# Kernel tuning notes

Measured on AMD Instinct MI355X. Metric: run time of the kernel, lower is better.

The kernel has to match this reference:

```python
import jax, jax.numpy as jnp
import numpy as np

N_NODES = 50000


def gcn_conv(h, src, dst, W, b, n):
    # PyG GCNConv: x' = D^{-1/2} (A + I) D^{-1/2} (h W) + b
    x = h @ W  # [N, out]
    deg = jax.ops.segment_sum(jnp.ones_like(src, dtype=x.dtype), dst, num_segments=n) + 1.0  # self-loop
    dis = deg ** -0.5
    norm = dis[src] * dis[dst]  # [E]
    msg = x[src] * norm[:, None]  # [E, out]
    agg = jax.ops.segment_sum(msg, dst, num_segments=n)
    agg = agg + x * (dis * dis)[:, None]  # self-loop term: 1/deg_i * x_i
    return agg + b


def setup_inputs() -> dict:
    key = jax.random.key(0)
    ks = jax.random.split(key, 8)
    n, e = N_NODES, 800000
    d_in, d_rni, h = 128, 32, 256
    x = jax.random.normal(ks[0], (n, d_in), dtype=jnp.float32)
    rni = jax.random.normal(ks[1], (n, d_rni), dtype=jnp.float32)
    edge_index = jax.random.randint(ks[2], (2, e), 0, n, dtype=jnp.int64)
    s1 = (d_in + d_rni) ** -0.5
    s2 = h ** -0.5
    W1 = jax.random.normal(ks[3], (d_in + d_rni, h), dtype=jnp.float32) * s1
    b1 = jnp.zeros((h,), dtype=jnp.float32)
    W2 = jax.random.normal(ks[4], (h, h), dtype=jnp.float32) * s2
    b2 = jnp.zeros((h,), dtype=jnp.float32)
    W_out = jax.random.normal(ks[5], (h, h), dtype=jnp.float32) * s2
    b_out = jnp.zeros((h,), dtype=jnp.float32)
    return {"x": x, "rni": rni, "edge_index": edge_index, "W1": W1, "b1": b1,
            "W2": W2, "b2": b2, "W_out": W_out, "b_out": b_out}


def reference(x, rni, edge_index, W1, b1, W2, b2, W_out, b_out):
    n = x.shape[0]
    src, dst = edge_index[0], edge_index[1]
    h = jnp.concatenate([x, rni], axis=-1)  # RNI concat
    h = jax.nn.relu(gcn_conv(h, src, dst, W1, b1, n))
    h = jax.nn.relu(gcn_conv(h, src, dst, W2, b2, n))
    return h @ W_out + b_out
```

## Files before the change

### kernel.cpp

```cpp
#include <hip/hip_runtime.h>
#include <hip/hip_bf16.h>
#include <hip/hip_fp16.h>
#include <math.h>

#define D_IN   128
#define D_RNI  32
#define HID    256

typedef _Float16 half8 __attribute__((ext_vector_type(8)));
typedef float    f32x4 __attribute__((ext_vector_type(4)));

__global__ void k_prep(const unsigned int* __restrict__ ew, int nwords, int* __restrict__ mode,
                       const float* __restrict__ W1, __half* __restrict__ W1t,
                       const float* __restrict__ W2, __half* __restrict__ W2t,
                       const float* __restrict__ Wo, __half* __restrict__ Wot,
                       int* __restrict__ counts, int n) {
    int b = blockIdx.x;
    if (b == 0) {
        __shared__ unsigned int red[256];
        unsigned int acc = 0;
        for (int i = threadIdx.x; i < 1024; i += 256) {
            int idx = 2 * i + 1;
            if (idx < nwords) acc |= ew[idx];
        }
        red[threadIdx.x] = acc;
        __syncthreads();
        for (int s = 128; s > 0; s >>= 1) {
            if (threadIdx.x < s) red[threadIdx.x] |= red[threadIdx.x + s];
            __syncthreads();
        }
        if (threadIdx.x == 0) *mode = (red[0] == 0u) ? 1 : 0;
        return;
    }
    const int T1 = (D_IN + D_RNI) * HID;
    const int T2 = HID * HID;
    const int TW = T1 + 2 * T2;
    int i = (b - 1) * 256 + threadIdx.x;
    if (i < T1) {
        int k = i / HID, nn = i - k * HID;
        W1t[(size_t)nn * (D_IN + D_RNI) + k] = __float2half(W1[i]);
    } else if (i < T1 + T2) {
        int j = i - T1;
        int k = j / HID, nn = j - k * HID;
        W2t[(size_t)nn * HID + k] = __float2half(W2[j]);
    } else if (i < TW) {
        int j = i - T1 - T2;
        int k = j / HID, nn = j - k * HID;
        Wot[(size_t)nn * HID + k] = __float2half(Wo[j]);
    } else {
        int j = i - TW;
        if (j < n) counts[j] = 0;
    }
}

__global__ void k_count(const unsigned int* __restrict__ ew, const int* __restrict__ mode_p,
                        int* __restrict__ counts, int e) {
    int mode = *mode_p;
    int i = blockIdx.x * 256 + threadIdx.x;
    if (i >= e) return;
    int d = mode ? (int)ew[2 * ((size_t)e + i)] : (int)ew[(size_t)e + i];
    atomicAdd(&counts[d], 1);
}

__global__ __launch_bounds__(1024) void k_scan1(const int* __restrict__ counts,
                                                int* __restrict__ incl,
                                                int* __restrict__ bsum, int n) {
    __shared__ int sd[1024];
    int t = threadIdx.x;
    int i = blockIdx.x * 1024 + t;
    int v = (i < n) ? counts[i] : 0;
    sd[t] = v;
    __syncthreads();
    for (int off = 1; off < 1024; off <<= 1) {
        int tmp = (t >= off) ? sd[t - off] : 0;
        __syncthreads();
        sd[t] += tmp;
        __syncthreads();
    }
    if (i < n) incl[i] = sd[t];
    if (t == 1023) bsum[blockIdx.x] = sd[1023];
}

__global__ void k_scan3(const int* __restrict__ counts, const int* __restrict__ incl,
                        const int* __restrict__ bsum,
                        int* __restrict__ rowptr, int* __restrict__ cursor,
                        float* __restrict__ dis, int n, int nb) {
    __shared__ int pre_s, tot_s;
    int t = threadIdx.x;
    int c = (blockIdx.x * 256) >> 10;
    if (t < 64) {
        int v   = (t < nb) ? bsum[t] : 0;
        int pre = (t < c)  ? v : 0;
        int tot = v;
        #pragma unroll
        for (int m = 32; m > 0; m >>= 1) {
            pre += __shfl_down(pre, m);
            tot += __shfl_down(tot, m);
        }
        if (t == 0) { pre_s = pre; tot_s = tot; }
    }
    __syncthreads();
    int i = blockIdx.x * 256 + t;
    if (i >= n) return;
    int excl = incl[i] - counts[i] + pre_s;
    rowptr[i] = excl;
    cursor[i] = excl;
    dis[i] = 1.0f / sqrtf((float)(counts[i] + 1));
    if (i == 0) rowptr[n] = tot_s;
}

#define KT 32
#define LSTR 40
template <bool A_F32, bool ADD_BIAS, bool HALF_OUT>
__device__ __forceinline__ void gemm_body(int blk,
                                          const void* __restrict__ Av, int strideA, int KA,
                                          const void* __restrict__ A2v, int strideA2,
                                          const __half* __restrict__ Bt,
                                          const float* __restrict__ bias,
                                          void* Cv, int M, int K) {
    __shared__ __half As[2][128 * LSTR];
    __shared__ __half Bs[2][256 * LSTR];
    int tid = threadIdx.x;
    int wave = tid >> 6, lane = tid & 63;
    int wm = wave >> 2, wn = wave & 3;
    int q = lane >> 4, m16 = lane & 15;
    int r0 = blk * 128;

    int ar  = tid >> 2, akq = (tid & 3) * 8;
    int br  = tid >> 1, bkq = (tid & 1) * 16;

    int arow = r0 + ar; if (arow >= M) arow = M - 1;

    f32x4 acc[4][4] = {};

    float4 afr0, afr1;
    uint4  areg;
    uint4  breg0, breg1;

    auto loadA = [&](int k0) {
        if (A_F32) {
            const float* src; int stride, kk0;
            if (k0 < KA) { src = (const float*)Av;  stride = strideA;  kk0 = k0; }
            else         { src = (const float*)A2v; stride = strideA2; kk0 = k0 - KA; }
            const float* p = &src[(size_t)arow * stride + kk0 + akq];
            afr0 = *reinterpret_cast<const float4*>(p);
            afr1 = *reinterpret_cast<const float4*>(p + 4);
        } else {
            const __half* src = (const __half*)Av;
            areg = *reinterpret_cast<const uint4*>(&src[(size_t)arow * strideA + k0 + akq]);
        }
    };
    auto loadB = [&](int k0) {
        const __half* p = &Bt[(size_t)br * K + k0 + bkq];
        breg0 = *reinterpret_cast<const uint4*>(p);
        breg1 = *reinterpret_cast<const uint4*>(p + 8);
    };
    auto writeLDS = [&](int buf) {
        if (A_F32) {
            union { __half2 h2[4]; uint4 u; } uu;
            uu.h2[0] = __floats2half2_rn(afr0.x, afr0.y);
            uu.h2[1] = __floats2half2_rn(afr0.z, afr0.w);
            uu.h2[2] = __floats2half2_rn(afr1.x, afr1.y);
            uu.h2[3] = __floats2half2_rn(afr1.z, afr1.w);
            *reinterpret_cast<uint4*>(&As[buf][ar * LSTR + akq]) = uu.u;
        } else {
            *reinterpret_cast<uint4*>(&As[buf][ar * LSTR + akq]) = areg;
        }
        *reinterpret_cast<uint4*>(&Bs[buf][br * LSTR + bkq])     = breg0;
        *reinterpret_cast<uint4*>(&Bs[buf][br * LSTR + bkq + 8]) = breg1;
    };

    const int S = K / KT;
    loadA(0); loadB(0);
    writeLDS(0);
    __syncthreads();

    for (int t = 0; t < S; ++t) {
        int cur = t & 1;
        if (t + 1 < S) { loadA((t + 1) * KT); loadB((t + 1) * KT); }

        half8 af[4], bf[4];
        #pragma unroll
        for (int mi = 0; mi < 4; ++mi)
            af[mi] = *reinterpret_cast<const half8*>(&As[cur][(wm * 64 + mi * 16 + m16) * LSTR + q * 8]);
        #pragma unroll
        for (int ni = 0; ni < 4; ++ni)
            bf[ni] = *reinterpret_cast<const half8*>(&Bs[cur][(wn * 64 + ni * 16 + m16) * LSTR + q * 8]);
        #pragma unroll
        for (int mi = 0; mi < 4; ++mi)
            #pragma unroll
            for (int ni = 0; ni < 4; ++ni)
                acc[mi][ni] = __builtin_amdgcn_mfma_f32_16x16x32_f16(af[mi], bf[ni], acc[mi][ni], 0, 0, 0);

        if (t + 1 < S) writeLDS(cur ^ 1);
        __syncthreads();
    }

    #pragma unroll
    for (int mi = 0; mi < 4; ++mi) {
        #pragma unroll
        for (int r = 0; r < 4; ++r) {
            int row = r0 + wm * 64 + mi * 16 + q * 4 + r;
            if (row >= M) continue;
            #pragma unroll
            for (int ni = 0; ni < 4; ++ni) {
                int col = wn * 64 + ni * 16 + m16;
                float v = acc[mi][ni][r];
                if (ADD_BIAS) v += bias[col];
                if (HALF_OUT) ((__half*)Cv)[(size_t)row * HID + col] = __float2half(v);
                else          ((float*)Cv)[(size_t)row * HID + col] = v;
            }
        }
    }
}

template <bool A_F32, bool ADD_BIAS, bool HALF_OUT>
__global__ __launch_bounds__(512, 4) void k_mgemm(const void* __restrict__ Av, int strideA, int KA,
                                                  const void* __restrict__ A2v, int strideA2,
                                                  const __half* __restrict__ Bt,
                                                  const float* __restrict__ bias,
                                                  void* Cv, int M, int K) {
    gemm_body<A_F32, ADD_BIAS, HALF_OUT>(blockIdx.x, Av, strideA, KA, A2v, strideA2,
                                         Bt, bias, Cv, M, K);
}

#define SCAT_BLKS 121
__global__ __launch_bounds__(512, 4) void k_scatgemm(
        const unsigned int* __restrict__ ew, const int* __restrict__ mode_p,
        int* __restrict__ cursor, int* __restrict__ csr, int e,
        const float* __restrict__ x, const float* __restrict__ rni,
        const __half* __restrict__ W1t, __half* __restrict__ xh, int M, int K) {
    if ((int)blockIdx.x >= SCAT_BLKS) {
        gemm_body<true, false, true>((int)blockIdx.x - SCAT_BLKS, x, D_IN, D_IN, rni, D_RNI,
                                     W1t, nullptr, xh, M, K);
        return;
    }
    const int t0     = (int)blockIdx.x * 512 + (int)threadIdx.x;
    const int stride = SCAT_BLKS * 512 * 4;
    const int mode   = *mode_p;
    for (int i = t0 * 4; i < e; i += stride) {
        if (i + 4 <= e) {
            int s0, s1, s2, s3, d0, d1, d2, d3;
            if (mode) {
                s0 = (int)ew[2 * (size_t)(i + 0)]; d0 = (int)ew[2 * ((size_t)e + i + 0)];
                s1 = (int)ew[2 * (size_t)(i + 1)]; d1 = (int)ew[2 * ((size_t)e + i + 1)];
                s2 = (int)ew[2 * (size_t)(i + 2)]; d2 = (int)ew[2 * ((size_t)e + i + 2)];
                s3 = (int)ew[2 * (size_t)(i + 3)]; d3 = (int)ew[2 * ((size_t)e + i + 3)];
            } else {
                s0 = (int)ew[(size_t)(i + 0)]; d0 = (int)ew[(size_t)e + i + 0];
                s1 = (int)ew[(size_t)(i + 1)]; d1 = (int)ew[(size_t)e + i + 1];
                s2 = (int)ew[(size_t)(i + 2)]; d2 = (int)ew[(size_t)e + i + 2];
                s3 = (int)ew[(size_t)(i + 3)]; d3 = (int)ew[(size_t)e + i + 3];
            }
            int p0 = atomicAdd(&cursor[d0], 1);
            int p1 = atomicAdd(&cursor[d1], 1);
            int p2 = atomicAdd(&cursor[d2], 1);
            int p3 = atomicAdd(&cursor[d3], 1);
            csr[p0] = s0; csr[p1] = s1; csr[p2] = s2; csr[p3] = s3;
        } else {
            for (int j = i; j < e; ++j) {
                int s, d;
                if (mode) { s = (int)ew[2 * (size_t)j]; d = (int)ew[2 * ((size_t)e + j)]; }
                else      { s = (int)ew[(size_t)j];     d = (int)ew[(size_t)e + j]; }
                int pos = atomicAdd(&cursor[d], 1);
                csr[pos] = s;
            }
        }
    }
}

__global__ __launch_bounds__(256) void k_agg(const __half* __restrict__ xh,
                                             const int* __restrict__ rowptr,
                                             const int* __restrict__ csr,
                                             const float* __restrict__ dis,
                                             const float* __restrict__ bias,
                                             __half* __restrict__ outh, int n) {
    int i = blockIdx.x * 4 + (threadIdx.x >> 6);
    if (i >= n) return;
    int lane = threadIdx.x & 63;
    int c4 = lane * 4;
    float disd = dis[i];
    int e0 = rowptr[i], e1 = rowptr[i + 1];

    float acc0, acc1, acc2, acc3;
    {
        uint2 v = *reinterpret_cast<const uint2*>(&xh[(size_t)i * HID + c4]);
        float2 f0 = __half22float2(*reinterpret_cast<__half2*>(&v.x));
        float2 f1 = __half22float2(*reinterpret_cast<__half2*>(&v.y));
        float ws = disd * disd;
        acc0 = f0.x * ws; acc1 = f0.y * ws; acc2 = f1.x * ws; acc3 = f1.y * ws;
    }

    for (int e = e0; e < e1; e += 64) {
        int cnt = min(64, e1 - e);
        int sreg = 0; float wreg = 0.0f;
        if (lane < cnt) {
            sreg = csr[e + lane];
            wreg = dis[sreg] * disd;
        }
        int j = 0;
        for (; j + 4 <= cnt; j += 4) {
            int   s0 = __shfl(sreg, j + 0), s1 = __shfl(sreg, j + 1);
            int   s2 = __shfl(sreg, j + 2), s3 = __shfl(sreg, j + 3);
            float w0 = __shfl(wreg, j + 0), w1 = __shfl(wreg, j + 1);
            float w2 = __shfl(wreg, j + 2), w3 = __shfl(wreg, j + 3);
            uint2 v0 = *reinterpret_cast<const uint2*>(&xh[(size_t)s0 * HID + c4]);
            uint2 v1 = *reinterpret_cast<const uint2*>(&xh[(size_t)s1 * HID + c4]);
            uint2 v2 = *reinterpret_cast<const uint2*>(&xh[(size_t)s2 * HID + c4]);
            uint2 v3 = *reinterpret_cast<const uint2*>(&xh[(size_t)s3 * HID + c4]);
            float2 a0 = __half22float2(*reinterpret_cast<__half2*>(&v0.x));
            float2 b0 = __half22float2(*reinterpret_cast<__half2*>(&v0.y));
            float2 a1 = __half22float2(*reinterpret_cast<__half2*>(&v1.x));
            float2 b1 = __half22float2(*reinterpret_cast<__half2*>(&v1.y));
            float2 a2 = __half22float2(*reinterpret_cast<__half2*>(&v2.x));
            float2 b2 = __half22float2(*reinterpret_cast<__half2*>(&v2.y));
            float2 a3 = __half22float2(*reinterpret_cast<__half2*>(&v3.x));
            float2 b3 = __half22float2(*reinterpret_cast<__half2*>(&v3.y));
            acc0 = fmaf(a0.x, w0, acc0); acc1 = fmaf(a0.y, w0, acc1);
            acc2 = fmaf(b0.x, w0, acc2); acc3 = fmaf(b0.y, w0, acc3);
            acc0 = fmaf(a1.x, w1, acc0); acc1 = fmaf(a1.y, w1, acc1);
            acc2 = fmaf(b1.x, w1, acc2); acc3 = fmaf(b1.y, w1, acc3);
            acc0 = fmaf(a2.x, w2, acc0); acc1 = fmaf(a2.y, w2, acc1);
            acc2 = fmaf(b2.x, w2, acc2); acc3 = fmaf(b2.y, w2, acc3);
            acc0 = fmaf(a3.x, w3, acc0); acc1 = fmaf(a3.y, w3, acc1);
            acc2 = fmaf(b3.x, w3, acc2); acc3 = fmaf(b3.y, w3, acc3);
        }
        for (; j < cnt; ++j) {
            int   s = __shfl(sreg, j);
            float w = __shfl(wreg, j);
            uint2 v = *reinterpret_cast<const uint2*>(&xh[(size_t)s * HID + c4]);
            float2 a = __half22float2(*reinterpret_cast<__half2*>(&v.x));
            float2 b = __half22float2(*reinterpret_cast<__half2*>(&v.y));
            acc0 = fmaf(a.x, w, acc0); acc1 = fmaf(a.y, w, acc1);
            acc2 = fmaf(b.x, w, acc2); acc3 = fmaf(b.y, w, acc3);
        }
    }

    float4 bb = *reinterpret_cast<const float4*>(&bias[c4]);
    union { __half2 h2[2]; uint2 u; } o;
    o.h2[0] = __floats2half2_rn(fmaxf(acc0 + bb.x, 0.0f), fmaxf(acc1 + bb.y, 0.0f));
    o.h2[1] = __floats2half2_rn(fmaxf(acc2 + bb.z, 0.0f), fmaxf(acc3 + bb.w, 0.0f));
    *reinterpret_cast<uint2*>(&outh[(size_t)i * HID + c4]) = o.u;
}

extern "C" void kernel_launch(void* const* d_in, const int* in_sizes, int n_in,
                              void* d_out, int out_size, void* d_ws, size_t ws_size,
                              hipStream_t stream) {
    const float* x     = (const float*)d_in[0];
    const float* rni   = (const float*)d_in[1];
    const unsigned int* ew = (const unsigned int*)d_in[2];
    const float* W1    = (const float*)d_in[3];
    const float* b1    = (const float*)d_in[4];
    const float* W2    = (const float*)d_in[5];
    const float* b2    = (const float*)d_in[6];
    const float* W_out = (const float*)d_in[7];
    const float* b_out = (const float*)d_in[8];
    float* out = (float*)d_out;

    const int n  = in_sizes[0] / D_IN;
    const int e  = in_sizes[2] / 2;
    const int nb = (n + 1023) / 1024;
    const int K1 = D_IN + D_RNI;

    char* ws = (char*)d_ws;
    size_t off = 0;
    auto carve = [&](size_t bytes) {
        char* p = ws + off;
        off = (off + bytes + 255) & ~(size_t)255;
        return p;
    };
    __half* xh    = (__half*)carve((size_t)n * HID * sizeof(__half));
    __half* h     = (__half*)carve((size_t)n * HID * sizeof(__half));
    __half* W1t   = (__half*)carve((size_t)K1 * HID * sizeof(__half));
    __half* W2t   = (__half*)carve((size_t)HID * HID * sizeof(__half));
    __half* Wot   = (__half*)carve((size_t)HID * HID * sizeof(__half));
    int*   counts = (int*)carve((size_t)n * sizeof(int));
    int*   incl   = (int*)carve((size_t)n * sizeof(int));
    int*   bsum   = (int*)carve((size_t)(nb + 1) * sizeof(int));
    int*   rowptr = (int*)carve((size_t)(n + 1) * sizeof(int));
    int*   cursor = (int*)carve((size_t)n * sizeof(int));
    float* dis    = (float*)carve((size_t)n * sizeof(float));
    int*   csr    = (int*)carve((size_t)e * sizeof(int));
    int*   mode   = (int*)carve(sizeof(int));
    (void)ws_size;

    const int eb = (e + 255) / 256;
    const int gemm_blocks = (n + 127) / 128;
    const int agg_blocks  = (n + 3) / 4;
    const int TW = K1 * HID + 2 * HID * HID;
    const int prep_blocks = 1 + (TW + n + 255) / 256;

    k_prep<<<prep_blocks, 256, 0, stream>>>(ew, 2 * e, mode, W1, W1t, W2, W2t, W_out, Wot,
                                            counts, n);
    k_count<<<eb, 256, 0, stream>>>(ew, mode, counts, e);
    k_scan1<<<nb, 1024, 0, stream>>>(counts, incl, bsum, n);
    k_scan3<<<(n + 255) / 256, 256, 0, stream>>>(counts, incl, bsum, rowptr, cursor, dis, n, nb);

    k_scatgemm<<<SCAT_BLKS + gemm_blocks, 512, 0, stream>>>(ew, mode, cursor, csr, e,
                                                            x, rni, W1t, xh, n, K1);
    k_agg<<<agg_blocks, 256, 0, stream>>>(xh, rowptr, csr, dis, b1, h, n);

    k_mgemm<false, false, true><<<gemm_blocks, 512, 0, stream>>>(h, HID, HID, nullptr, 0,
                                                                 W2t, nullptr, xh, n, HID);
    k_agg<<<agg_blocks, 256, 0, stream>>>(xh, rowptr, csr, dis, b2, h, n);

    k_mgemm<false, true, false><<<gemm_blocks, 512, 0, stream>>>(h, HID, HID, nullptr, 0,
                                                                 Wot, b_out, out, n, HID);
}
```

Before: 343.7 us.

## Split node range in halves to overlap aggregation with dense GEMM

Splits each aggregation+GEMM stage into two halves by node range. A combined kernel runs the GEMM on the first half concurrently with aggregation of the second half, aiming to overlap the memory-bound gather with the MFMA-bound GEMM. A single-buffered LDS variant of the GEMM body is added for the fused kernel to cut shared memory so both block types can co-reside. An extra activation buffer is introduced, and the launch count goes up.

Result: slower. 361.8 us (+5.3%).

```diff
diff --git a/kernel.cpp b/kernel.cpp
--- a/kernel.cpp
+++ b/kernel.cpp
@@ -111,15 +111,16 @@
 
 #define KT 32
 #define LSTR 40
-template <bool A_F32, bool ADD_BIAS, bool HALF_OUT>
+template <bool A_F32, bool ADD_BIAS, bool HALF_OUT, bool DBUF>
 __device__ __forceinline__ void gemm_body(int blk,
                                           const void* __restrict__ Av, int strideA, int KA,
                                           const void* __restrict__ A2v, int strideA2,
                                           const __half* __restrict__ Bt,
                                           const float* __restrict__ bias,
                                           void* Cv, int M, int K) {
-    __shared__ __half As[2][128 * LSTR];
-    __shared__ __half Bs[2][256 * LSTR];
+    constexpr int NB = DBUF ? 2 : 1;
+    __shared__ __half As[NB * 128 * LSTR];
+    __shared__ __half Bs[NB * 256 * LSTR];
     int tid = threadIdx.x;
     int wave = tid >> 6, lane = tid & 63;
     int wm = wave >> 2, wn = wave & 3;
@@ -162,38 +163,51 @@
             uu.h2[1] = __floats2half2_rn(afr0.z, afr0.w);
             uu.h2[2] = __floats2half2_rn(afr1.x, afr1.y);
             uu.h2[3] = __floats2half2_rn(afr1.z, afr1.w);
-            *reinterpret_cast<uint4*>(&As[buf][ar * LSTR + akq]) = uu.u;
+            *reinterpret_cast<uint4*>(&As[buf * (128 * LSTR) + ar * LSTR + akq]) = uu.u;
         } else {
-            *reinterpret_cast<uint4*>(&As[buf][ar * LSTR + akq]) = areg;
-        }
-        *reinterpret_cast<uint4*>(&Bs[buf][br * LSTR + bkq])     = breg0;
-        *reinterpret_cast<uint4*>(&Bs[buf][br * LSTR + bkq + 8]) = breg1;
+            *reinterpret_cast<uint4*>(&As[buf * (128 * LSTR) + ar * LSTR + akq]) = areg;
+        }
+        *reinterpret_cast<uint4*>(&Bs[buf * (256 * LSTR) + br * LSTR + bkq])     = breg0;
+        *reinterpret_cast<uint4*>(&Bs[buf * (256 * LSTR) + br * LSTR + bkq + 8]) = breg1;
     };
-
-    const int S = K / KT;
-    loadA(0); loadB(0);
-    writeLDS(0);
-    __syncthreads();
-
-    for (int t = 0; t < S; ++t) {
-        int cur = t & 1;
-        if (t + 1 < S) { loadA((t + 1) * KT); loadB((t + 1) * KT); }
-
+    auto compute = [&](int buf) {
         half8 af[4], bf[4];
         #pragma unroll
         for (int mi = 0; mi < 4; ++mi)
-            af[mi] = *reinterpret_cast<const half8*>(&As[cur][(wm * 64 + mi * 16 + m16) * LSTR + q * 8]);
+            af[mi] = *reinterpret_cast<const half8*>(
+                &As[buf * (128 * LSTR) + (wm * 64 + mi * 16 + m16) * LSTR + q * 8]);
         #pragma unroll
         for (int ni = 0; ni < 4; ++ni)
-            bf[ni] = *reinterpret_cast<const half8*>(&Bs[cur][(wn * 64 + ni * 16 + m16) * LSTR + q * 8]);
+            bf[ni] = *reinterpret_cast<const half8*>(
+                &Bs[buf * (256 * LSTR) + (wn * 64 + ni * 16 + m16) * LSTR + q * 8]);
         #pragma unroll
         for (int mi = 0; mi < 4; ++mi)
             #pragma unroll
             for (int ni = 0; ni < 4; ++ni)
                 acc[mi][ni] = __builtin_amdgcn_mfma_f32_16x16x32_f16(af[mi], bf[ni], acc[mi][ni], 0, 0, 0);
-
-        if (t + 1 < S) writeLDS(cur ^ 1);
+    };
+
+    const int S = K / KT;
+    if (DBUF) {
+        loadA(0); loadB(0);
+        writeLDS(0);
         __syncthreads();
+        for (int t = 0; t < S; ++t) {
+            int cur = t & 1;
+            if (t + 1 < S) { loadA((t + 1) * KT); loadB((t + 1) * KT); }
+            compute(cur);
+            if (t + 1 < S) writeLDS(cur ^ 1);
+            __syncthreads();
+        }
+    } else {
+        loadA(0); loadB(0);
+        for (int t = 0; t < S; ++t) {
+            __syncthreads();
+            writeLDS(0);
+            __syncthreads();
+            if (t + 1 < S) { loadA((t + 1) * KT); loadB((t + 1) * KT); }
+            compute(0);
+        }
     }
 
     #pragma unroll
@@ -220,8 +234,107 @@
                                                   const __half* __restrict__ Bt,
                                                   const float* __restrict__ bias,
                                                   void* Cv, int M, int K) {
-    gemm_body<A_F32, ADD_BIAS, HALF_OUT>(blockIdx.x, Av, strideA, KA, A2v, strideA2,
-                                         Bt, bias, Cv, M, K);
+    gemm_body<A_F32, ADD_BIAS, HALF_OUT, true>(blockIdx.x, Av, strideA, KA, A2v, strideA2,
+                                               Bt, bias, Cv, M, K);
+}
+
+__device__ __forceinline__ void agg_node(int i,
+                                         const __half* __restrict__ xh,
+                                         const int* __restrict__ rowptr,
+                                         const int* __restrict__ csr,
+                                         const float* __restrict__ dis,
+                                         const float* __restrict__ bias,
+                                         __half* __restrict__ outh) {
+    int lane = threadIdx.x & 63;
+    int c4 = lane * 4;
+    float disd = dis[i];
+    int e0 = rowptr[i], e1 = rowptr[i + 1];
+
+    float acc0, acc1, acc2, acc3;
+    {
+        uint2 v = *reinterpret_cast<const uint2*>(&xh[(size_t)i * HID + c4]);
+        float2 f0 = __half22float2(*reinterpret_cast<__half2*>(&v.x));
+        float2 f1 = __half22float2(*reinterpret_cast<__half2*>(&v.y));
+        float ws = disd * disd;
+        acc0 = f0.x * ws; acc1 = f0.y * ws; acc2 = f1.x * ws; acc3 = f1.y * ws;
+    }
+
+    for (int e = e0; e < e1; e += 64) {
+        int cnt = min(64, e1 - e);
+        int sreg = 0; float wreg = 0.0f;
+        if (lane < cnt) {
+            sreg = csr[e + lane];
+            wreg = dis[sreg] * disd;
+        }
+        int j = 0;
+        for (; j + 4 <= cnt; j += 4) {
+            int   s0 = __shfl(sreg, j + 0), s1 = __shfl(sreg, j + 1);
+            int   s2 = __shfl(sreg, j + 2), s3 = __shfl(sreg, j + 3);
+            float w0 = __shfl(wreg, j + 0), w1 = __shfl(wreg, j + 1);
+            float w2 = __shfl(wreg, j + 2), w3 = __shfl(wreg, j + 3);
+            uint2 v0 = *reinterpret_cast<const uint2*>(&xh[(size_t)s0 * HID + c4]);
+            uint2 v1 = *reinterpret_cast<const uint2*>(&xh[(size_t)s1 * HID + c4]);
+            uint2 v2 = *reinterpret_cast<const uint2*>(&xh[(size_t)s2 * HID + c4]);
+            uint2 v3 = *reinterpret_cast<const uint2*>(&xh[(size_t)s3 * HID + c4]);
+            float2 a0 = __half22float2(*reinterpret_cast<__half2*>(&v0.x));
+            float2 b0 = __half22float2(*reinterpret_cast<__half2*>(&v0.y));
+            float2 a1 = __half22float2(*reinterpret_cast<__half2*>(&v1.x));
+            float2 b1 = __half22float2(*reinterpret_cast<__half2*>(&v1.y));
+            float2 a2 = __half22float2(*reinterpret_cast<__half2*>(&v2.x));
+            float2 b2 = __half22float2(*reinterpret_cast<__half2*>(&v2.y));
+            float2 a3 = __half22float2(*reinterpret_cast<__half2*>(&v3.x));
+            float2 b3 = __half22float2(*reinterpret_cast<__half2*>(&v3.y));
+            acc0 = fmaf(a0.x, w0, acc0); acc1 = fmaf(a0.y, w0, acc1);
+            acc2 = fmaf(b0.x, w0, acc2); acc3 = fmaf(b0.y, w0, acc3);
+            acc0 = fmaf(a1.x, w1, acc0); acc1 = fmaf(a1.y, w1, acc1);
+            acc2 = fmaf(b1.x, w1, acc2); acc3 = fmaf(b1.y, w1, acc3);
+            acc0 = fmaf(a2.x, w2, acc0); acc1 = fmaf(a2.y, w2, acc1);
+            acc2 = fmaf(b2.x, w2, acc2); acc3 = fmaf(b2.y, w2, acc3);
+            acc0 = fmaf(a3.x, w3, acc0); acc1 = fmaf(a3.y, w3, acc1);
+            acc2 = fmaf(b3.x, w3, acc2); acc3 = fmaf(b3.y, w3, acc3);
+        }
+        for (; j < cnt; ++j) {
+            int   s = __shfl(sreg, j);
+            float w = __shfl(wreg, j);
+            uint2 v = *reinterpret_cast<const uint2*>(&xh[(size_t)s * HID + c4]);
+            float2 a = __half22float2(*reinterpret_cast<__half2*>(&v.x));
+            float2 b = __half22float2(*reinterpret_cast<__half2*>(&v.y));
+            acc0 = fmaf(a.x, w, acc0); acc1 = fmaf(a.y, w, acc1);
+            acc2 = fmaf(b.x, w, acc2); acc3 = fmaf(b.y, w, acc3);
+        }
+    }
+
+    float4 bb = *reinterpret_cast<const float4*>(&bias[c4]);
+    union { __half2 h2[2]; uint2 u; } o;
+    o.h2[0] = __floats2half2_rn(fmaxf(acc0 + bb.x, 0.0f), fmaxf(acc1 + bb.y, 0.0f));
+    o.h2[1] = __floats2half2_rn(fmaxf(acc2 + bb.z, 0.0f), fmaxf(acc3 + bb.w, 0.0f));
+    *reinterpret_cast<uint2*>(&outh[(size_t)i * HID + c4]) = o.u;
+}
+
+__global__ __launch_bounds__(256) void k_agg(const __half* __restrict__ xh,
+                                             const int* __restrict__ rowptr,
+                                             const int* __restrict__ csr,
+                                             const float* __restrict__ dis,
+                                             const float* __restrict__ bias,
+                                             __half* __restrict__ outh, int i0, int i1) {
+    int i = i0 + blockIdx.x * 4 + (threadIdx.x >> 6);
+    if (i < i1) agg_node(i, xh, rowptr, csr, dis, bias, outh);
+}
+
+template <bool ADD_BIAS_G, bool HALF_OUT_G>
+__global__ __launch_bounds__(512, 4) void k_aggemm(
+        const __half* __restrict__ Ag, const __half* __restrict__ Btg,
+        const float* __restrict__ biasg, void* Cg, int Mg, int G,
+        const __half* __restrict__ xa, const int* __restrict__ rowptr,
+        const int* __restrict__ csr, const float* __restrict__ dis,
+        const float* __restrict__ biasa, __half* __restrict__ outa, int i0, int i1) {
+    if ((int)blockIdx.x < G) {
+        gemm_body<false, ADD_BIAS_G, HALF_OUT_G, false>(blockIdx.x, Ag, HID, HID, nullptr, 0,
+                                                        Btg, biasg, Cg, Mg, HID);
+        return;
+    }
+    int i = i0 + ((int)blockIdx.x - G) * 8 + ((int)threadIdx.x >> 6);
+    if (i < i1) agg_node(i, xa, rowptr, csr, dis, biasa, outa);
 }
 
 #define SCAT_BLKS 121
@@ -231,8 +344,8 @@
         const float* __restrict__ x, const float* __restrict__ rni,
         const __half* __restrict__ W1t, __half* __restrict__ xh, int M, int K) {
     if ((int)blockIdx.x >= SCAT_BLKS) {
-        gemm_body<true, false, true>((int)blockIdx.x - SCAT_BLKS, x, D_IN, D_IN, rni, D_RNI,
-                                     W1t, nullptr, xh, M, K);
+        gemm_body<true, false, true, true>((int)blockIdx.x - SCAT_BLKS, x, D_IN, D_IN, rni, D_RNI,
+                                           W1t, nullptr, xh, M, K);
         return;
     }
     const int t0     = (int)blockIdx.x * 512 + (int)threadIdx.x;
@@ -269,80 +382,6 @@
     }
 }
 
-__global__ __launch_bounds__(256) void k_agg(const __half* __restrict__ xh,
-                                             const int* __restrict__ rowptr,
-                                             const int* __restrict__ csr,
-                                             const float* __restrict__ dis,
-                                             const float* __restrict__ bias,
-                                             __half* __restrict__ outh, int n) {
-    int i = blockIdx.x * 4 + (threadIdx.x >> 6);
-    if (i >= n) return;
-    int lane = threadIdx.x & 63;
-    int c4 = lane * 4;
-    float disd = dis[i];
-    int e0 = rowptr[i], e1 = rowptr[i + 1];
-
-    float acc0, acc1, acc2, acc3;
-    {
-        uint2 v = *reinterpret_cast<const uint2*>(&xh[(size_t)i * HID + c4]);
-        float2 f0 = __half22float2(*reinterpret_cast<__half2*>(&v.x));
-        float2 f1 = __half22float2(*reinterpret_cast<__half2*>(&v.y));
-        float ws = disd * disd;
-        acc0 = f0.x * ws; acc1 = f0.y * ws; acc2 = f1.x * ws; acc3 = f1.y * ws;
-    }
-
-    for (int e = e0; e < e1; e += 64) {
-        int cnt = min(64, e1 - e);
-        int sreg = 0; float wreg = 0.0f;
-        if (lane < cnt) {
-            sreg = csr[e + lane];
-            wreg = dis[sreg] * disd;
-        }
-        int j = 0;
-        for (; j + 4 <= cnt; j += 4) {
-            int   s0 = __shfl(sreg, j + 0), s1 = __shfl(sreg, j + 1);
-            int   s2 = __shfl(sreg, j + 2), s3 = __shfl(sreg, j + 3);
-            float w0 = __shfl(wreg, j + 0), w1 = __shfl(wreg, j + 1);
-            float w2 = __shfl(wreg, j + 2), w3 = __shfl(wreg, j + 3);
-            uint2 v0 = *reinterpret_cast<const uint2*>(&xh[(size_t)s0 * HID + c4]);
-            uint2 v1 = *reinterpret_cast<const uint2*>(&xh[(size_t)s1 * HID + c4]);
-            uint2 v2 = *reinterpret_cast<const uint2*>(&xh[(size_t)s2 * HID + c4]);
-            uint2 v3 = *reinterpret_cast<const uint2*>(&xh[(size_t)s3 * HID + c4]);
-            float2 a0 = __half22float2(*reinterpret_cast<__half2*>(&v0.x));
-            float2 b0 = __half22float2(*reinterpret_cast<__half2*>(&v0.y));
-            float2 a1 = __half22float2(*reinterpret_cast<__half2*>(&v1.x));
-            float2 b1 = __half22float2(*reinterpret_cast<__half2*>(&v1.y));
-            float2 a2 = __half22float2(*reinterpret_cast<__half2*>(&v2.x));
-            float2 b2 = __half22float2(*reinterpret_cast<__half2*>(&v2.y));
-            float2 a3 = __half22float2(*reinterpret_cast<__half2*>(&v3.x));
-            float2 b3 = __half22float2(*reinterpret_cast<__half2*>(&v3.y));
-            acc0 = fmaf(a0.x, w0, acc0); acc1 = fmaf(a0.y, w0, acc1);
-            acc2 = fmaf(b0.x, w0, acc2); acc3 = fmaf(b0.y, w0, acc3);
-            acc0 = fmaf(a1.x, w1, acc0); acc1 = fmaf(a1.y, w1, acc1);
-            acc2 = fmaf(b1.x, w1, acc2); acc3 = fmaf(b1.y, w1, acc3);
-            acc0 = fmaf(a2.x, w2, acc0); acc1 = fmaf(a2.y, w2, acc1);
-            acc2 = fmaf(b2.x, w2, acc2); acc3 = fmaf(b2.y, w2, acc3);
-            acc0 = fmaf(a3.x, w3, acc0); acc1 = fmaf(a3.y, w3, acc1);
-            acc2 = fmaf(b3.x, w3, acc2); acc3 = fmaf(b3.y, w3, acc3);
-        }
-        for (; j < cnt; ++j) {
-            int   s = __shfl(sreg, j);
-            float w = __shfl(wreg, j);
-            uint2 v = *reinterpret_cast<const uint2*>(&xh[(size_t)s * HID + c4]);
-            float2 a = __half22float2(*reinterpret_cast<__half2*>(&v.x));
-            float2 b = __half22float2(*reinterpret_cast<__half2*>(&v.y));
-            acc0 = fmaf(a.x, w, acc0); acc1 = fmaf(a.y, w, acc1);
-            acc2 = fmaf(b.x, w, acc2); acc3 = fmaf(b.y, w, acc3);
-        }
-    }
-
-    float4 bb = *reinterpret_cast<const float4*>(&bias[c4]);
-    union { __half2 h2[2]; uint2 u; } o;
-    o.h2[0] = __floats2half2_rn(fmaxf(acc0 + bb.x, 0.0f), fmaxf(acc1 + bb.y, 0.0f));
-    o.h2[1] = __floats2half2_rn(fmaxf(acc2 + bb.z, 0.0f), fmaxf(acc3 + bb.w, 0.0f));
-    *reinterpret_cast<uint2*>(&outh[(size_t)i * HID + c4]) = o.u;
-}
-
 extern "C" void kernel_launch(void* const* d_in, const int* in_sizes, int n_in,
                               void* d_out, int out_size, void* d_ws, size_t ws_size,
                               hipStream_t stream) {
@@ -371,6 +410,7 @@
     };
     __half* xh    = (__half*)carve((size_t)n * HID * sizeof(__half));
     __half* h     = (__half*)carve((size_t)n * HID * sizeof(__half));
+    __half* xh2   = (__half*)carve((size_t)n * HID * sizeof(__half));
     __half* W1t   = (__half*)carve((size_t)K1 * HID * sizeof(__half));
     __half* W2t   = (__half*)carve((size_t)HID * HID * sizeof(__half));
     __half* Wot   = (__half*)carve((size_t)HID * HID * sizeof(__half));
@@ -386,9 +426,15 @@
 
     const int eb = (e + 255) / 256;
     const int gemm_blocks = (n + 127) / 128;
-    const int agg_blocks  = (n + 3) / 4;
     const int TW = K1 * HID + 2 * HID * HID;
     const int prep_blocks = 1 + (TW + n + 255) / 256;
+
+    int half = ((n / 2 + 127) / 128) * 128;
+    if (half > n) half = (n / 128) * 128;
+    const int G2      = half / 128;
+    const int aggH0b  = (half + 3) / 4;
+    const int aggH1b  = (n - half + 7) / 8;
+    const int gH1b    = (n - half + 127) / 128;
 
     k_prep<<<prep_blocks, 256, 0, stream>>>(ew, 2 * e, mode, W1, W1t, W2, W2t, W_out, Wot,
                                             counts, n);
@@ -398,12 +444,20 @@
 
     k_scatgemm<<<SCAT_BLKS + gemm_blocks, 512, 0, stream>>>(ew, mode, cursor, csr, e,
                                                             x, rni, W1t, xh, n, K1);
-    k_agg<<<agg_blocks, 256, 0, stream>>>(xh, rowptr, csr, dis, b1, h, n);
-
-    k_mgemm<false, false, true><<<gemm_blocks, 512, 0, stream>>>(h, HID, HID, nullptr, 0,
-                                                                 W2t, nullptr, xh, n, HID);
-    k_agg<<<agg_blocks, 256, 0, stream>>>(xh, rowptr, csr, dis, b2, h, n);
-
-    k_mgemm<false, true, false><<<gemm_blocks, 512, 0, stream>>>(h, HID, HID, nullptr, 0,
-                                                                 Wot, b_out, out, n, HID);
-}
+
+    k_agg<<<aggH0b, 256, 0, stream>>>(xh, rowptr, csr, dis, b1, h, 0, half);
+    k_aggemm<false, true><<<G2 + aggH1b, 512, 0, stream>>>(
+        h, W2t, nullptr, xh2, half, G2,
+        xh, rowptr, csr, dis, b1, h, half, n);
+    k_mgemm<false, false, true><<<gH1b, 512, 0, stream>>>(
+        h + (size_t)half * HID, HID, HID, nullptr, 0, W2t, nullptr,
+        xh2 + (size_t)half * HID, n - half, HID);
+
+    k_agg<<<aggH0b, 256, 0, stream>>>(xh2, rowptr, csr, dis, b2, xh, 0, half);
+    k_aggemm<true, false><<<G2 + aggH1b, 512, 0, stream>>>(
+        xh, Wot, b_out, out, half, G2,
+        xh2, rowptr, csr, dis, b2, xh, half, n);
+    k_mgemm<false, true, false><<<gH1b, 512, 0, stream>>>(
+        xh + (size_t)half * HID, HID, HID, nullptr, 0, Wot, b_out,
+        out + (size_t)half * HID, n - half, HID);
+}
```

## Replace LDS double-buffered GEMM with register-direct MFMA GEMM on 64-row tiles

Applied to the files above, without the earlier changes.

The shared-memory staged, double-buffered GEMM (128x256 tile, 512 threads) is replaced by a kernel that loads A and B fragments straight from global memory into registers for MFMA. K is now a template parameter so the loop fully unrolls, and blocks shrink to 64 rows and 256 threads. This removes LDS traffic and barriers. In exchange, each of the four waves reloads the same A rows, B is re-read per block from cache, and there is no explicit prefetch to hide global latency. The scatter portion of the fused kernel is re-split across 242 blocks of 256 threads.

After: 390.6 us. 13.6% more time.

```diff
diff --git a/kernel.cpp b/kernel.cpp
--- a/kernel.cpp
+++ b/kernel.cpp
@@ -110,97 +110,69 @@
 }
 
 #define KT 32
-#define LSTR 40
-template <bool A_F32, bool ADD_BIAS, bool HALF_OUT>
-__device__ __forceinline__ void gemm_body(int blk,
-                                          const void* __restrict__ Av, int strideA, int KA,
-                                          const void* __restrict__ A2v, int strideA2,
-                                          const __half* __restrict__ Bt,
-                                          const float* __restrict__ bias,
-                                          void* Cv, int M, int K) {
-    __shared__ __half As[2][128 * LSTR];
-    __shared__ __half Bs[2][256 * LSTR];
+template <bool A_F32, bool ADD_BIAS, bool HALF_OUT, int K>
+__device__ __forceinline__ void sgemm_body(int blk,
+                                           const void* __restrict__ Av, int strideA, int KA,
+                                           const void* __restrict__ A2v, int strideA2,
+                                           const __half* __restrict__ Bt,
+                                           const float* __restrict__ bias,
+                                           void* Cv, int M) {
     int tid = threadIdx.x;
-    int wave = tid >> 6, lane = tid & 63;
-    int wm = wave >> 2, wn = wave & 3;
+    int wn = tid >> 6, lane = tid & 63;
     int q = lane >> 4, m16 = lane & 15;
-    int r0 = blk * 128;
-
-    int ar  = tid >> 2, akq = (tid & 3) * 8;
-    int br  = tid >> 1, bkq = (tid & 1) * 16;
-
-    int arow = r0 + ar; if (arow >= M) arow = M - 1;
+    int r0 = blk * 64;
+
+    int arow[4];
+    #pragma unroll
+    for (int mi = 0; mi < 4; ++mi) {
+        int r = r0 + mi * 16 + m16;
+        arow[mi] = (r < M) ? r : (M - 1);
+    }
 
     f32x4 acc[4][4] = {};
 
-    float4 afr0, afr1;
-    uint4  areg;
-    uint4  breg0, breg1;
-
-    auto loadA = [&](int k0) {
+    #pragma unroll
+    for (int k0 = 0; k0 < K; k0 += KT) {
+        half8 af[4], bf[4];
         if (A_F32) {
-            const float* src; int stride, kk0;
-            if (k0 < KA) { src = (const float*)Av;  stride = strideA;  kk0 = k0; }
-            else         { src = (const float*)A2v; stride = strideA2; kk0 = k0 - KA; }
-            const float* p = &src[(size_t)arow * stride + kk0 + akq];
-            afr0 = *reinterpret_cast<const float4*>(p);
-            afr1 = *reinterpret_cast<const float4*>(p + 4);
+            #pragma unroll
+            for (int mi = 0; mi < 4; ++mi) {
+                const float* src; int stride, kk0;
+                if (k0 < KA) { src = (const float*)Av;  stride = strideA;  kk0 = k0; }
+                else         { src = (const float*)A2v; stride = strideA2; kk0 = k0 - KA; }
+                const float* p = &src[(size_t)arow[mi] * stride + kk0 + q * 8];
+                float4 va = *reinterpret_cast<const float4*>(p);
+                float4 vb = *reinterpret_cast<const float4*>(p + 4);
+                union { __half2 h2[4]; half8 h8; } uu;
+                uu.h2[0] = __floats2half2_rn(va.x, va.y);
+                uu.h2[1] = __floats2half2_rn(va.z, va.w);
+                uu.h2[2] = __floats2half2_rn(vb.x, vb.y);
+                uu.h2[3] = __floats2half2_rn(vb.z, vb.w);
+                af[mi] = uu.h8;
+            }
         } else {
             const __half* src = (const __half*)Av;
-            areg = *reinterpret_cast<const uint4*>(&src[(size_t)arow * strideA + k0 + akq]);
-        }
-    };
-    auto loadB = [&](int k0) {
-        const __half* p = &Bt[(size_t)br * K + k0 + bkq];
-        breg0 = *reinterpret_cast<const uint4*>(p);
-        breg1 = *reinterpret_cast<const uint4*>(p + 8);
-    };
-    auto writeLDS = [&](int buf) {
-        if (A_F32) {
-            union { __half2 h2[4]; uint4 u; } uu;
-            uu.h2[0] = __floats2half2_rn(afr0.x, afr0.y);
-            uu.h2[1] = __floats2half2_rn(afr0.z, afr0.w);
-            uu.h2[2] = __floats2half2_rn(afr1.x, afr1.y);
-            uu.h2[3] = __floats2half2_rn(afr1.z, afr1.w);
-            *reinterpret_cast<uint4*>(&As[buf][ar * LSTR + akq]) = uu.u;
-        } else {
-            *reinterpret_cast<uint4*>(&As[buf][ar * LSTR + akq]) = areg;
-        }
-        *reinterpret_cast<uint4*>(&Bs[buf][br * LSTR + bkq])     = breg0;
-        *reinterpret_cast<uint4*>(&Bs[buf][br * LSTR + bkq + 8]) = breg1;
-    };
-
-    const int S = K / KT;
-    loadA(0); loadB(0);
-    writeLDS(0);
-    __syncthreads();
-
-    for (int t = 0; t < S; ++t) {
-        int cur = t & 1;
-        if (t + 1 < S) { loadA((t + 1) * KT); loadB((t + 1) * KT); }
-
-        half8 af[4], bf[4];
-        #pragma unroll
-        for (int mi = 0; mi < 4; ++mi)
-            af[mi] = *reinterpret_cast<const half8*>(&As[cur][(wm * 64 + mi * 16 + m16) * LSTR + q * 8]);
+            #pragma unroll
+            for (int mi = 0; mi < 4; ++mi)
+                af[mi] = *reinterpret_cast<const half8*>(
+                    &src[(size_t)arow[mi] * strideA + k0 + q * 8]);
+        }
         #pragma unroll
         for (int ni = 0; ni < 4; ++ni)
-            bf[ni] = *reinterpret_cast<const half8*>(&Bs[cur][(wn * 64 + ni * 16 + m16) * LSTR + q * 8]);
+            bf[ni] = *reinterpret_cast<const half8*>(
+                &Bt[(size_t)(wn * 64 + ni * 16 + m16) * K + k0 + q * 8]);
         #pragma unroll
         for (int mi = 0; mi < 4; ++mi)
             #pragma unroll
             for (int ni = 0; ni < 4; ++ni)
                 acc[mi][ni] = __builtin_amdgcn_mfma_f32_16x16x32_f16(af[mi], bf[ni], acc[mi][ni], 0, 0, 0);
-
-        if (t + 1 < S) writeLDS(cur ^ 1);
-        __syncthreads();
     }
 
     #pragma unroll
     for (int mi = 0; mi < 4; ++mi) {
         #pragma unroll
         for (int r = 0; r < 4; ++r) {
-            int row = r0 + wm * 64 + mi * 16 + q * 4 + r;
+            int row = r0 + mi * 16 + q * 4 + r;
             if (row >= M) continue;
             #pragma unroll
             for (int ni = 0; ni < 4; ++ni) {
@@ -214,29 +186,29 @@
     }
 }
 
-template <bool A_F32, bool ADD_BIAS, bool HALF_OUT>
-__global__ __launch_bounds__(512, 4) void k_mgemm(const void* __restrict__ Av, int strideA, int KA,
+template <bool A_F32, bool ADD_BIAS, bool HALF_OUT, int K>
+__global__ __launch_bounds__(256, 4) void k_sgemm(const void* __restrict__ Av, int strideA, int KA,
                                                   const void* __restrict__ A2v, int strideA2,
                                                   const __half* __restrict__ Bt,
                                                   const float* __restrict__ bias,
-                                                  void* Cv, int M, int K) {
-    gemm_body<A_F32, ADD_BIAS, HALF_OUT>(blockIdx.x, Av, strideA, KA, A2v, strideA2,
-                                         Bt, bias, Cv, M, K);
-}
-
-#define SCAT_BLKS 121
-__global__ __launch_bounds__(512, 4) void k_scatgemm(
+                                                  void* Cv, int M) {
+    sgemm_body<A_F32, ADD_BIAS, HALF_OUT, K>(blockIdx.x, Av, strideA, KA, A2v, strideA2,
+                                             Bt, bias, Cv, M);
+}
+
+#define SCAT2 242
+__global__ __launch_bounds__(256, 4) void k_scatgemm(
         const unsigned int* __restrict__ ew, const int* __restrict__ mode_p,
         int* __restrict__ cursor, int* __restrict__ csr, int e,
         const float* __restrict__ x, const float* __restrict__ rni,
-        const __half* __restrict__ W1t, __half* __restrict__ xh, int M, int K) {
-    if ((int)blockIdx.x >= SCAT_BLKS) {
-        gemm_body<true, false, true>((int)blockIdx.x - SCAT_BLKS, x, D_IN, D_IN, rni, D_RNI,
-                                     W1t, nullptr, xh, M, K);
+        const __half* __restrict__ W1t, __half* __restrict__ xh, int M) {
+    if ((int)blockIdx.x >= SCAT2) {
+        sgemm_body<true, false, true, D_IN + D_RNI>((int)blockIdx.x - SCAT2, x, D_IN, D_IN,
+                                                    rni, D_RNI, W1t, nullptr, xh, M);
         return;
     }
-    const int t0     = (int)blockIdx.x * 512 + (int)threadIdx.x;
-    const int stride = SCAT_BLKS * 512 * 4;
+    const int t0     = (int)blockIdx.x * 256 + (int)threadIdx.x;
+    const int stride = SCAT2 * 256 * 4;
     const int mode   = *mode_p;
     for (int i = t0 * 4; i < e; i += stride) {
         if (i + 4 <= e) {
@@ -385,8 +357,8 @@
     (void)ws_size;
 
     const int eb = (e + 255) / 256;
-    const int gemm_blocks = (n + 127) / 128;
-    const int agg_blocks  = (n + 3) / 4;
+    const int g64 = (n + 63) / 64;
+    const int agg_blocks = (n + 3) / 4;
     const int TW = K1 * HID + 2 * HID * HID;
     const int prep_blocks = 1 + (TW + n + 255) / 256;
 
@@ -396,14 +368,14 @@
     k_scan1<<<nb, 1024, 0, stream>>>(counts, incl, bsum, n);
     k_scan3<<<(n + 255) / 256, 256, 0, stream>>>(counts, incl, bsum, rowptr, cursor, dis, n, nb);
 
-    k_scatgemm<<<SCAT_BLKS + gemm_blocks, 512, 0, stream>>>(ew, mode, cursor, csr, e,
-                                                            x, rni, W1t, xh, n, K1);
+    k_scatgemm<<<SCAT2 + g64, 256, 0, stream>>>(ew, mode, cursor, csr, e,
+                                                x, rni, W1t, xh, n);
     k_agg<<<agg_blocks, 256, 0, stream>>>(xh, rowptr, csr, dis, b1, h, n);
 
-    k_mgemm<false, false, true><<<gemm_blocks, 512, 0, stream>>>(h, HID, HID, nullptr, 0,
-                                                                 W2t, nullptr, xh, n, HID);
+    k_sgemm<false, false, true, HID><<<g64, 256, 0, stream>>>(h, HID, HID, nullptr, 0,
+                                                              W2t, nullptr, xh, n);
     k_agg<<<agg_blocks, 256, 0, stream>>>(xh, rowptr, csr, dis, b2, h, n);
 
-    k_mgemm<false, true, false><<<gemm_blocks, 512, 0, stream>>>(h, HID, HID, nullptr, 0,
-                                                                 Wot, b_out, out, n, HID);
-}
+    k_sgemm<false, true, false, HID><<<g64, 256, 0, stream>>>(h, HID, HID, nullptr, 0,
+                                                              Wot, b_out, out, n);
+}
```
